# Optimization experiments

Measured on AMD Instinct MI355X. Metric: run time of the kernel, lower is better.

The kernel has to match this reference:

```python
import jax, jax.numpy as jnp
import numpy as np

N, E, D, B = 50000, 800000, 64, 64
NEXP, NC, EDIM, PDIM = 4, 10, 4, 100


def setup_inputs() -> dict:
    key = jax.random.key(0)
    ks = jax.random.split(key, 24)
    s = lambda f: 1.0 / np.sqrt(f)
    inp = {
        'x': jax.random.normal(ks[0], (N, D), jnp.float32),
        'edge_index': jax.random.randint(ks[1], (2, E), 0, N, jnp.int32),
        'edge_attr': jax.random.normal(ks[2], (E, EDIM), jnp.float32),
        'batch': jnp.sort(jax.random.randint(ks[3], (N,), 0, B, jnp.int32)),
        'ldxb_flag': jax.random.normal(ks[4], (B,), jnp.float32),
        # layer 1 params
        'w_edge1': jax.random.normal(ks[5], (D, EDIM)) * s(EDIM),
        'b_edge1': jnp.zeros((D,), jnp.float32),
        'w_ih1': jax.random.normal(ks[6], (3 * D, D)) * s(D),
        'w_hh1': jax.random.normal(ks[7], (3 * D, D)) * s(D),
        'b_ih1': jnp.zeros((3 * D,), jnp.float32),
        'b_hh1': jnp.zeros((3 * D,), jnp.float32),
        # layer 2 params
        'w_edge2': jax.random.normal(ks[8], (D, EDIM)) * s(EDIM),
        'b_edge2': jnp.zeros((D,), jnp.float32),
        'w_ih2': jax.random.normal(ks[9], (3 * D, D)) * s(D),
        'w_hh2': jax.random.normal(ks[10], (3 * D, D)) * s(D),
        'b_ih2': jnp.zeros((3 * D,), jnp.float32),
        'b_hh2': jnp.zeros((3 * D,), jnp.float32),
        # MoE
        'gate_w': jax.random.normal(ks[11], (NEXP, D)) * s(D),
        'gate_b': jnp.zeros((NEXP,), jnp.float32),
        'exp_w': jax.random.normal(ks[12], (NEXP, D, D)) * s(D),
        'exp_b': jnp.zeros((NEXP, D), jnp.float32),
        # heads
        'proj_w': jax.random.normal(ks[13], (PDIM, 1)),
        'proj_b': jnp.zeros((PDIM,), jnp.float32),
        'fc_w': jax.random.normal(ks[14], (NC, D + PDIM)) * s(D + PDIM),
        'fc_b': jnp.zeros((NC,), jnp.float32),
    }
    return inp


def _ggnn_layer(x, src, dst, eemb, w_ih, w_hh, b_ih, b_hh):
    # gather + scatter-add message passing (self-loops already in src/dst/eemb)
    msg = x[src] + eemb                       # [E+N, D]
    m = jnp.zeros_like(x).at[dst].add(msg)    # [N, D]
    # GRUCell(m, x): x is the hidden state
    gi = m @ w_ih.T + b_ih
    gh = x @ w_hh.T + b_hh
    i_r, i_z, i_n = jnp.split(gi, 3, axis=1)
    h_r, h_z, h_n = jnp.split(gh, 3, axis=1)
    r = jax.nn.sigmoid(i_r + h_r)
    z = jax.nn.sigmoid(i_z + h_z)
    n = jnp.tanh(i_n + r * h_n)
    return (1.0 - z) * n + z * x


def reference(x, edge_index, edge_attr, batch, ldxb_flag,
              w_edge1, b_edge1, w_ih1, w_hh1, b_ih1, b_hh1,
              w_edge2, b_edge2, w_ih2, w_hh2, b_ih2, b_hh2,
              gate_w, gate_b, exp_w, exp_b, proj_w, proj_b, fc_w, fc_b):
    n = x.shape[0]
    loop = jnp.arange(n, dtype=edge_index.dtype)
    src = jnp.concatenate([edge_index[0], loop])
    dst = jnp.concatenate([edge_index[1], loop])
    ea = jnp.concatenate([edge_attr, jnp.zeros((n, edge_attr.shape[1]), edge_attr.dtype)], axis=0)

    h = _ggnn_layer(x, src, dst, ea @ w_edge1.T + b_edge1, w_ih1, w_hh1, b_ih1, b_hh1)
    h = jax.nn.relu(h)
    h = _ggnn_layer(h, src, dst, ea @ w_edge2.T + b_edge2, w_ih2, w_hh2, b_ih2, b_hh2)
    h = jax.nn.relu(h)

    # soft MoE combine
    gw = jax.nn.softmax(h @ gate_w.T + gate_b, axis=1)            # [N, NEXP]
    eo = jax.nn.relu(jnp.einsum('nd,ehd->neh', h, exp_w) + exp_b)  # [N, NEXP, D]
    h = jnp.einsum('ne,neh->nh', gw, eo)                           # [N, D]

    # global mean pool per graph
    sums = jax.ops.segment_sum(h, batch, num_segments=B)
    cnts = jax.ops.segment_sum(jnp.ones((n,), h.dtype), batch, num_segments=B)
    graph_emb = sums / jnp.maximum(cnts, 1.0)[:, None]             # [B, D]

    flag = ldxb_flag[:, None] @ proj_w.T + proj_b                  # [B, 100]
    logits = jnp.concatenate([flag, graph_emb], axis=1) @ fc_w.T + fc_b
    return (graph_emb, graph_emb, logits)
```

## Files before the change

kernel.cpp:

```cpp
#include <hip/hip_runtime.h>
#include <stdint.h>


#define SUBCAP 8
#define OVF_MAX 32768
#define PS 16

typedef __bf16 bf16x8 __attribute__((ext_vector_type(8)));
typedef float floatx4 __attribute__((ext_vector_type(4)));
typedef unsigned short us8 __attribute__((ext_vector_type(8)));

__device__ __forceinline__ unsigned short f2bf(float f){
  union { float f; unsigned u; } c; c.f = f;
  unsigned r = c.u + 0x7FFFu + ((c.u >> 16) & 1u);
  return (unsigned short)(r >> 16);
}
__device__ __forceinline__ float bf2f(unsigned short u){
  union { unsigned u; float f; } c; c.u = ((unsigned)u) << 16; return c.f;
}
__device__ __forceinline__ float sigm(float x){ return 1.f/(1.f + __expf(-x)); }

__global__ void k_init(const float* __restrict__ x, unsigned short* __restrict__ x_bf,
                       const float* __restrict__ s0, const float* __restrict__ s1,
                       const float* __restrict__ s2, const float* __restrict__ s3,
                       const float* __restrict__ s4, const float* __restrict__ s5,
                       unsigned short* __restrict__ dst,
                       int* __restrict__ cur, int* __restrict__ ovfcnt,
                       int nTot, int N8){
  int i = blockIdx.x*blockDim.x + threadIdx.x;
  if (i < nTot) x_bf[i] = f2bf(x[i]);
  if (i < N8) cur[i] = 0;
  if (i == 0){ ovfcnt[0] = 0; }
  if (i >= 65792) return;
  const float* s; int off;
  if      (i < 12288){ s = s0; off = i; }
  else if (i < 24576){ s = s1; off = i - 12288; }
  else if (i < 36864){ s = s2; off = i - 24576; }
  else if (i < 49152){ s = s3; off = i - 36864; }
  else if (i < 49408){ s = s4; off = i - 49152; }
  else               { s = s5; off = i - 49408; }
  dst[i] = f2bf(s[off]);
}

__global__ void k_bucket(const int* __restrict__ ei, const float* __restrict__ ea,
                         int* __restrict__ cur, int4* __restrict__ bkt,
                         int* __restrict__ ovfcnt, int* __restrict__ ovf,
                         int E, int N){
  int base = (blockIdx.x*blockDim.x + threadIdx.x)*2;
  if (base >= E) return;
  int sub = blockIdx.x & 7;
  bool v1 = base + 1 < E;
  int2 ss = *(const int2*)(ei + base);
  int2 dd = *(const int2*)(ei + E + base);
  if (!v1){ dd.y = dd.x; ss.y = ss.x; }
  float4 a0 = *(const float4*)(ea + (size_t)base*4);
  float4 a1 = v1 ? *(const float4*)(ea + (size_t)(base+1)*4) : a0;
  size_t sb0 = (size_t)sub*N + dd.x;
  size_t sb1 = (size_t)sub*N + dd.y;
  int p0 = atomicAdd(&cur[sb0], 1);
  int p1 = v1 ? atomicAdd(&cur[sb1], 1) : SUBCAP;
  if (p0 < SUBCAP){
    int4 rec;
    rec.x = ss.x;
    rec.y = (int)((unsigned)f2bf(a0.x) | ((unsigned)f2bf(a0.y) << 16));
    rec.z = (int)((unsigned)f2bf(a0.z) | ((unsigned)f2bf(a0.w) << 16));
    rec.w = 0;
    bkt[sb0*SUBCAP + p0] = rec;
  } else {
    int o = atomicAdd(ovfcnt, 1);
    if (o < OVF_MAX) ovf[o] = base;
  }
  if (v1){
    if (p1 < SUBCAP){
      int4 rec;
      rec.x = ss.y;
      rec.y = (int)((unsigned)f2bf(a1.x) | ((unsigned)f2bf(a1.y) << 16));
      rec.z = (int)((unsigned)f2bf(a1.z) | ((unsigned)f2bf(a1.w) << 16));
      rec.w = 0;
      bkt[sb1*SUBCAP + p1] = rec;
    } else {
      int o = atomicAdd(ovfcnt, 1);
      if (o < OVF_MAX) ovf[o] = base + 1;
    }
  }
}

__global__ void __launch_bounds__(256) k_gather(
    const int* __restrict__ cur, const int4* __restrict__ bkt,
    const unsigned short* __restrict__ xbf,
    const float* __restrict__ w_edge, const float* __restrict__ b_edge,
    float* __restrict__ m, int N){
  int n = (int)(((long long)blockIdx.x*blockDim.x + threadIdx.x) >> 6);
  if (n >= N) return;
  int d = threadIdx.x & 63;
  int sub = d >> 3, k = d & 7;
  size_t sb = (size_t)sub*N + n;
  int myc = cur[sb];
  int contrib = (k == 0) ? myc : 0;
#pragma unroll
  for (int off = 1; off < 64; off <<= 1) contrib += __shfl_xor(contrib, off);
  int degAll = contrib;

  bool valid = k < min(myc, SUBCAP);
  int src = 0;
  float esx = 0.f, esy = 0.f, esz = 0.f, esw = 0.f;
  if (valid){
    int4 rec = bkt[sb*SUBCAP + k];
    src = rec.x;
    esx = bf2f((unsigned short)(rec.y      ));
    esy = bf2f((unsigned short)(rec.y >> 16));
    esz = bf2f((unsigned short)(rec.z      ));
    esw = bf2f((unsigned short)(rec.z >> 16));
  }

  float4 wv = *(const float4*)(w_edge + d*4);
  float acc = bf2f(xbf[(size_t)n*64 + d]) + (float)(degAll + 1) * b_edge[d];

  unsigned long long mm = __ballot(valid);
  while (mm){
    int l0 = (int)__builtin_ctzll(mm); mm &= mm - 1;
    int s0 = __shfl(src, l0);
    float a0 = bf2f(xbf[(size_t)s0*64 + d]);
    float a1 = 0.f, a2 = 0.f, a3 = 0.f;
    if (mm){
      int l1 = (int)__builtin_ctzll(mm); mm &= mm - 1;
      int s1 = __shfl(src, l1);
      a1 = bf2f(xbf[(size_t)s1*64 + d]);
      if (mm){
        int l2 = (int)__builtin_ctzll(mm); mm &= mm - 1;
        int s2 = __shfl(src, l2);
        a2 = bf2f(xbf[(size_t)s2*64 + d]);
        if (mm){
          int l3 = (int)__builtin_ctzll(mm); mm &= mm - 1;
          int s3 = __shfl(src, l3);
          a3 = bf2f(xbf[(size_t)s3*64 + d]);
        }
      }
    }
    acc += (a0 + a1) + (a2 + a3);
  }

#pragma unroll
  for (int off = 1; off < 64; off <<= 1){
    esx += __shfl_xor(esx, off);
    esy += __shfl_xor(esy, off);
    esz += __shfl_xor(esz, off);
    esw += __shfl_xor(esw, off);
  }
  acc += esx*wv.x + esy*wv.y + esz*wv.z + esw*wv.w;
  m[(size_t)n*64 + d] = acc;
}

__global__ void k_ovf(const int* __restrict__ ei, const float* __restrict__ ea,
                      const float* __restrict__ xin, const float* __restrict__ w_edge,
                      const int* __restrict__ ovf, const int* __restrict__ ovfcnt,
                      float* __restrict__ m, int E){
  int cnt = *ovfcnt; if (cnt > OVF_MAX) cnt = OVF_MAX;
  int nwaves = (gridDim.x * blockDim.x) >> 6;
  int wid = (int)((blockIdx.x*blockDim.x + threadIdx.x) >> 6);
  int d = threadIdx.x & 63;
  for (int k = wid; k < cnt; k += nwaves){
    int e = ovf[k];
    int s = ei[e], dst = ei[E + e];
    float4 v  = *(const float4*)(ea + (size_t)e*4);
    float4 wv = *(const float4*)(w_edge + d*4);
    float msg = xin[(size_t)s*64 + d] + v.x*wv.x + v.y*wv.y + v.z*wv.z + v.w*wv.w;
    atomicAdd(&m[(size_t)dst*64 + d], msg);
  }
}

__global__ void __launch_bounds__(256) k_gru(
    const float* __restrict__ m, const float* x,
    const unsigned short* __restrict__ xbf,
    const unsigned short* __restrict__ wih, const unsigned short* __restrict__ whh,
    const float* __restrict__ b_ih, const float* __restrict__ b_hh,
    float* out, unsigned short* out_bf, int tiles, int N){
  int wid = (int)(((long long)blockIdx.x*blockDim.x + threadIdx.x) >> 6);
  if (wid >= tiles) return;
  int lane = threadIdx.x & 63;
  int col = lane & 15, quad = lane >> 4;
  int na = wid*16 + col; if (na > N-1) na = N-1;

  bf16x8 am[2], ax[2];
#pragma unroll
  for (int ks = 0; ks < 2; ++ks){
    int kb = ks*32 + quad*8;
    const float4* mp = (const float4*)(m + (size_t)na*64 + kb);
    float4 lo = mp[0], hi = mp[1];
    us8 tm;
    tm[0]=f2bf(lo.x); tm[1]=f2bf(lo.y); tm[2]=f2bf(lo.z); tm[3]=f2bf(lo.w);
    tm[4]=f2bf(hi.x); tm[5]=f2bf(hi.y); tm[6]=f2bf(hi.z); tm[7]=f2bf(hi.w);
    am[ks] = __builtin_bit_cast(bf16x8, tm);
    ax[ks] = __builtin_bit_cast(bf16x8, *(const us8*)(xbf + (size_t)na*64 + kb));
  }

  floatx4 ai[12], ah[12];
#pragma unroll
  for (int nt = 0; nt < 12; ++nt){ ai[nt] = (floatx4)0.f; ah[nt] = (floatx4)0.f; }
#pragma unroll
  for (int nt = 0; nt < 12; ++nt){
    int r = nt*16 + col;
#pragma unroll
    for (int ks = 0; ks < 2; ++ks){
      int kb = ks*32 + quad*8;
      bf16x8 bi = __builtin_bit_cast(bf16x8, *(const us8*)(wih + (size_t)r*64 + kb));
      ai[nt] = __builtin_amdgcn_mfma_f32_16x16x32_bf16(am[ks], bi, ai[nt], 0,0,0);
      bf16x8 bh = __builtin_bit_cast(bf16x8, *(const us8*)(whh + (size_t)r*64 + kb));
      ah[nt] = __builtin_amdgcn_mfma_f32_16x16x32_bf16(ax[ks], bh, ah[nt], 0,0,0);
    }
  }

#pragma unroll
  for (int nt = 0; nt < 4; ++nt){
    int d = nt*16 + col;
    float bir = b_ih[d],      bhr = b_hh[d];
    float biz = b_ih[64+d],   bhz = b_hh[64+d];
    float bin = b_ih[128+d],  bhn = b_hh[128+d];
#pragma unroll
    for (int rg = 0; rg < 4; ++rg){
      int node = wid*16 + quad*4 + rg;
      if (node >= N) continue;
      float rr = sigm(ai[nt  ][rg] + bir + ah[nt  ][rg] + bhr);
      float zz = sigm(ai[nt+4][rg] + biz + ah[nt+4][rg] + bhz);
      float nn = tanhf(ai[nt+8][rg] + bin + rr*(ah[nt+8][rg] + bhn));
      float xv = x[(size_t)node*64 + d];
      float hv = fmaxf((1.f - zz)*nn + zz*xv, 0.f);
      out[(size_t)node*64 + d] = hv;
      out_bf[(size_t)node*64 + d] = f2bf(hv);
    }
  }
}

__global__ void __launch_bounds__(256) k_moe(
    const unsigned short* __restrict__ hbf,
    const unsigned short* __restrict__ gate_w, const float* __restrict__ gate_b,
    const unsigned short* __restrict__ exp_w,  const float* __restrict__ exp_b,
    float* __restrict__ v_out, int tiles, int N){
  __shared__ float gsm[4][16][4];
  int gwid = (int)(((long long)blockIdx.x*blockDim.x + threadIdx.x) >> 6);
  int w = threadIdx.x >> 6;
  int lane = threadIdx.x & 63;
  int col = lane & 15, quad = lane >> 4;
  bool active = gwid < tiles;

  floatx4 accg = (floatx4)0.f;
  floatx4 acce[4][4];
#pragma unroll
  for (int e=0;e<4;++e)
#pragma unroll
    for (int nt=0;nt<4;++nt) acce[e][nt] = (floatx4)0.f;

  if (active){
    int na = gwid*16 + col; if (na > N-1) na = N-1;
    bf16x8 a[2];
#pragma unroll
    for (int ks=0; ks<2; ++ks){
      int kb = ks*32 + quad*8;
      a[ks] = __builtin_bit_cast(bf16x8, *(const us8*)(hbf + (size_t)na*64 + kb));
      us8 braw = {0,0,0,0,0,0,0,0};
      if (col < 4) braw = *(const us8*)(gate_w + col*64 + kb);
      accg = __builtin_amdgcn_mfma_f32_16x16x32_bf16(a[ks], __builtin_bit_cast(bf16x8, braw), accg, 0,0,0);
    }
#pragma unroll
    for (int e=0;e<4;++e)
#pragma unroll
      for (int nt=0;nt<4;++nt)
#pragma unroll
        for (int ks=0;ks<2;++ks){
          int kb = ks*32 + quad*8;
          bf16x8 b = __builtin_bit_cast(bf16x8,
              *(const us8*)(exp_w + ((size_t)e*64 + nt*16 + col)*64 + kb));
          acce[e][nt] = __builtin_amdgcn_mfma_f32_16x16x32_bf16(a[ks], b, acce[e][nt], 0,0,0);
        }
    if (col < 4){
      float gb = gate_b[col];
#pragma unroll
      for (int rg=0;rg<4;++rg) gsm[w][quad*4+rg][col] = accg[rg] + gb;
    }
  }
  __syncthreads();
  if (!active) return;

#pragma unroll
  for (int rg=0; rg<4; ++rg){
    int nrow = quad*4 + rg;
    int node = gwid*16 + nrow;
    if (node >= N) continue;
    float g0=gsm[w][nrow][0], g1=gsm[w][nrow][1], g2=gsm[w][nrow][2], g3=gsm[w][nrow][3];
    float mx = fmaxf(fmaxf(g0,g1), fmaxf(g2,g3));
    float e0=__expf(g0-mx), e1=__expf(g1-mx), e2=__expf(g2-mx), e3=__expf(g3-mx);
    float inv = 1.f/(e0+e1+e2+e3);
    float w0=e0*inv, w1=e1*inv, w2=e2*inv, w3=e3*inv;
#pragma unroll
    for (int nt=0;nt<4;++nt){
      int o = nt*16 + col;
      float v = w0*fmaxf(acce[0][nt][rg] + exp_b[      o], 0.f)
              + w1*fmaxf(acce[1][nt][rg] + exp_b[ 64 + o], 0.f)
              + w2*fmaxf(acce[2][nt][rg] + exp_b[128 + o], 0.f)
              + w3*fmaxf(acce[3][nt][rg] + exp_b[192 + o], 0.f);
      v_out[(size_t)node*64 + o] = v;
    }
  }
}

__device__ __forceinline__ int lower_bound_i(const int* __restrict__ a, int n, int key){
  int lo = 0, hi = n;
  while (lo < hi){ int mid = (lo + hi) >> 1; if (a[mid] < key) lo = mid + 1; else hi = mid; }
  return lo;
}

__global__ void __launch_bounds__(256) k_pool(
    const float* __restrict__ v, const int* __restrict__ batch, int N,
    float* __restrict__ partial){
  __shared__ float red[4][64];
  int g = blockIdx.x / PS, s = blockIdx.x % PS;
  int t = threadIdx.x, d = t & 63, r = t >> 6;
  int start = lower_bound_i(batch, N, g);
  int end   = lower_bound_i(batch, N, g + 1);
  int len = end - start;
  int per = (len + PS - 1) / PS;
  int s0 = start + s*per;
  int s1 = s0 + per; if (s1 > end) s1 = end;
  float acc = 0.f;
  for (int i = s0 + r; i < s1; i += 4)
    acc += v[(size_t)i*64 + d];
  red[r][d] = acc;
  __syncthreads();
  if (r == 0)
    partial[(size_t)blockIdx.x*64 + d] = red[0][d] + red[1][d] + red[2][d] + red[3][d];
}

__global__ void __launch_bounds__(64) k_head(
    const float* __restrict__ partial, const int* __restrict__ batch, int N, int B,
    const float* __restrict__ ldxb,
    const float* __restrict__ proj_w, const float* __restrict__ proj_b,
    const float* __restrict__ fc_w, const float* __restrict__ fc_b,
    float* __restrict__ out){
  __shared__ float ges[64];
  int b = blockIdx.x, d = threadIdx.x;
  int start = lower_bound_i(batch, N, b);
  int end   = lower_bound_i(batch, N, b + 1);
  float sum = 0.f;
#pragma unroll
  for (int s = 0; s < PS; ++s)
    sum += partial[((size_t)b*PS + s)*64 + d];
  float ge = sum / fmaxf((float)(end - start), 1.f);
  ges[d] = ge;
  out[(size_t)b*64 + d]                = ge;
  out[(size_t)B*64 + (size_t)b*64 + d] = ge;
  __syncthreads();
  if (d < 10){
    float acc = fc_b[d];
    float fl = ldxb[b];
    const float* fr = fc_w + d*164;
    for (int p = 0; p < 100; ++p) acc += (fl*proj_w[p] + proj_b[p]) * fr[p];
    for (int dd = 0; dd < 64; ++dd) acc += ges[dd]*fr[100 + dd];
    out[(size_t)B*128 + (size_t)b*10 + d] = acc;
  }
}

extern "C" void kernel_launch(void* const* d_in, const int* in_sizes, int n_in,
                              void* d_out, int out_size, void* d_ws, size_t ws_size,
                              hipStream_t stream){
  const float* x      = (const float*)d_in[0];
  const int*   ei     = (const int*)d_in[1];
  const float* ea     = (const float*)d_in[2];
  const int*   batch  = (const int*)d_in[3];
  const float* ldxb   = (const float*)d_in[4];
  const float* w_edge1= (const float*)d_in[5];
  const float* b_edge1= (const float*)d_in[6];
  const float* w_ih1  = (const float*)d_in[7];
  const float* w_hh1  = (const float*)d_in[8];
  const float* b_ih1  = (const float*)d_in[9];
  const float* b_hh1  = (const float*)d_in[10];
  const float* w_edge2= (const float*)d_in[11];
  const float* b_edge2= (const float*)d_in[12];
  const float* w_ih2  = (const float*)d_in[13];
  const float* w_hh2  = (const float*)d_in[14];
  const float* b_ih2  = (const float*)d_in[15];
  const float* b_hh2  = (const float*)d_in[16];
  const float* gate_w = (const float*)d_in[17];
  const float* gate_b = (const float*)d_in[18];
  const float* exp_w  = (const float*)d_in[19];
  const float* exp_b  = (const float*)d_in[20];
  const float* proj_w = (const float*)d_in[21];
  const float* proj_b = (const float*)d_in[22];
  const float* fc_w   = (const float*)d_in[23];
  const float* fc_b   = (const float*)d_in[24];
  float* out = (float*)d_out;

  int N = in_sizes[0] / 64;
  int E = in_sizes[1] / 2;
  int B = in_sizes[4];
  int tiles = (N + 15) / 16;
  int nTot = N * 64;

  float*   m       = (float*)d_ws;
  float*   h       = m + (size_t)nTot;
  unsigned short* x_bf = (unsigned short*)(h + (size_t)nTot);
  unsigned short* h_bf = x_bf + (size_t)nTot;
  int4*    bkt     = (int4*)(h_bf + (size_t)nTot);
  int*     cur     = (int*)(bkt + (size_t)N*8*SUBCAP);
  int*     ovfcnt  = cur + (size_t)N*8;
  int*     ovf     = ovfcnt + 4;
  unsigned short* wbf = (unsigned short*)(ovf + OVF_MAX);
  float*   partial = (float*)(wbf + 65792);
  unsigned short* wih1bf = wbf;
  unsigned short* whh1bf = wbf + 12288;
  unsigned short* wih2bf = wbf + 24576;
  unsigned short* whh2bf = wbf + 36864;
  unsigned short* gatebf = wbf + 49152;
  unsigned short* expbf  = wbf + 49408;

  dim3 blk(256);
  int edgePairBlocks = (((E + 1)/2) + 255)/256;
  int nodeWaveBlocks = (N + 3)/4;
  int waveBlocks = (tiles + 3)/4;
  int N8 = N*8;
  int initMax = nTot > N8 ? nTot : N8; if (initMax < 65792) initMax = 65792;
  int initBlocks = (initMax + 255)/256;

  k_init<<<initBlocks, blk, 0, stream>>>(x, x_bf, w_ih1, w_hh1, w_ih2, w_hh2,
                                         gate_w, exp_w, wbf, cur, ovfcnt, nTot, N8);
  k_bucket<<<edgePairBlocks, blk, 0, stream>>>(ei, ea, cur, bkt, ovfcnt, ovf, E, N);
  k_gather<<<nodeWaveBlocks, blk, 0, stream>>>(cur, bkt, x_bf, w_edge1, b_edge1, m, N);
  k_ovf<<<64, blk, 0, stream>>>(ei, ea, x, w_edge1, ovf, ovfcnt, m, E);
  k_gru<<<waveBlocks, blk, 0, stream>>>(m, x, x_bf, wih1bf, whh1bf, b_ih1, b_hh1,
                                        h, h_bf, tiles, N);
  k_gather<<<nodeWaveBlocks, blk, 0, stream>>>(cur, bkt, h_bf, w_edge2, b_edge2, m, N);
  k_ovf<<<64, blk, 0, stream>>>(ei, ea, h, w_edge2, ovf, ovfcnt, m, E);
  k_gru<<<waveBlocks, blk, 0, stream>>>(m, h, h_bf, wih2bf, whh2bf, b_ih2, b_hh2,
                                        h, h_bf, tiles, N);
  k_moe<<<waveBlocks, blk, 0, stream>>>(h_bf, gatebf, gate_b, expbf, exp_b, m, tiles, N);
  k_pool<<<B*PS, blk, 0, stream>>>(m, batch, N, partial);
  k_head<<<B, 64, 0, stream>>>(partial, batch, N, B, ldxb, proj_w, proj_b, fc_w, fc_b, out);
}
```

Baseline: 369.2 us.

## Fold overflow edges into gather kernel and widen gather unroll to eight

The bucket kernel now writes self-contained overflow records (dst, src, packed bf16 edge attributes) instead of edge indices. Each gather wave scans the overflow list and adds any matching edges itself. This removes the separate atomic-based overflow kernel and its two launches. The gather loop also issues up to eight independent source-row loads per iteration instead of four, to expose more memory-level parallelism. In exchange, every node wave rereads the whole overflow list, and overflow messages now use bf16 features rather than fp32.

```diff
diff --git a/kernel.cpp b/kernel.cpp
--- a/kernel.cpp
+++ b/kernel.cpp
@@ -44,7 +44,7 @@
 
 __global__ void k_bucket(const int* __restrict__ ei, const float* __restrict__ ea,
                          int* __restrict__ cur, int4* __restrict__ bkt,
-                         int* __restrict__ ovfcnt, int* __restrict__ ovf,
+                         int* __restrict__ ovfcnt, int4* __restrict__ ovfrec,
                          int E, int N){
   int base = (blockIdx.x*blockDim.x + threadIdx.x)*2;
   if (base >= E) return;
@@ -59,28 +59,22 @@
   size_t sb1 = (size_t)sub*N + dd.y;
   int p0 = atomicAdd(&cur[sb0], 1);
   int p1 = v1 ? atomicAdd(&cur[sb1], 1) : SUBCAP;
+  int ea0_01 = (int)((unsigned)f2bf(a0.x) | ((unsigned)f2bf(a0.y) << 16));
+  int ea0_23 = (int)((unsigned)f2bf(a0.z) | ((unsigned)f2bf(a0.w) << 16));
   if (p0 < SUBCAP){
-    int4 rec;
-    rec.x = ss.x;
-    rec.y = (int)((unsigned)f2bf(a0.x) | ((unsigned)f2bf(a0.y) << 16));
-    rec.z = (int)((unsigned)f2bf(a0.z) | ((unsigned)f2bf(a0.w) << 16));
-    rec.w = 0;
-    bkt[sb0*SUBCAP + p0] = rec;
+    bkt[sb0*SUBCAP + p0] = make_int4(ss.x, ea0_01, ea0_23, 0);
   } else {
     int o = atomicAdd(ovfcnt, 1);
-    if (o < OVF_MAX) ovf[o] = base;
+    if (o < OVF_MAX) ovfrec[o] = make_int4(dd.x, ss.x, ea0_01, ea0_23);
   }
   if (v1){
+    int ea1_01 = (int)((unsigned)f2bf(a1.x) | ((unsigned)f2bf(a1.y) << 16));
+    int ea1_23 = (int)((unsigned)f2bf(a1.z) | ((unsigned)f2bf(a1.w) << 16));
     if (p1 < SUBCAP){
-      int4 rec;
-      rec.x = ss.y;
-      rec.y = (int)((unsigned)f2bf(a1.x) | ((unsigned)f2bf(a1.y) << 16));
-      rec.z = (int)((unsigned)f2bf(a1.z) | ((unsigned)f2bf(a1.w) << 16));
-      rec.w = 0;
-      bkt[sb1*SUBCAP + p1] = rec;
+      bkt[sb1*SUBCAP + p1] = make_int4(ss.y, ea1_01, ea1_23, 0);
     } else {
       int o = atomicAdd(ovfcnt, 1);
-      if (o < OVF_MAX) ovf[o] = base + 1;
+      if (o < OVF_MAX) ovfrec[o] = make_int4(dd.y, ss.y, ea1_01, ea1_23);
     }
   }
 }
@@ -89,6 +83,7 @@
     const int* __restrict__ cur, const int4* __restrict__ bkt,
     const unsigned short* __restrict__ xbf,
     const float* __restrict__ w_edge, const float* __restrict__ b_edge,
+    const int4* __restrict__ ovfrec, const int* __restrict__ ovfcnt,
     float* __restrict__ m, int N){
   int n = (int)(((long long)blockIdx.x*blockDim.x + threadIdx.x) >> 6);
   if (n >= N) return;
@@ -118,26 +113,24 @@
 
   unsigned long long mm = __ballot(valid);
   while (mm){
-    int l0 = (int)__builtin_ctzll(mm); mm &= mm - 1;
-    int s0 = __shfl(src, l0);
-    float a0 = bf2f(xbf[(size_t)s0*64 + d]);
-    float a1 = 0.f, a2 = 0.f, a3 = 0.f;
-    if (mm){
-      int l1 = (int)__builtin_ctzll(mm); mm &= mm - 1;
-      int s1 = __shfl(src, l1);
-      a1 = bf2f(xbf[(size_t)s1*64 + d]);
-      if (mm){
-        int l2 = (int)__builtin_ctzll(mm); mm &= mm - 1;
-        int s2 = __shfl(src, l2);
-        a2 = bf2f(xbf[(size_t)s2*64 + d]);
-        if (mm){
-          int l3 = (int)__builtin_ctzll(mm); mm &= mm - 1;
-          int s3 = __shfl(src, l3);
-          a3 = bf2f(xbf[(size_t)s3*64 + d]);
-        }
-      }
-    }
-    acc += (a0 + a1) + (a2 + a3);
+    int s0=-1,s1=-1,s2=-1,s3=-1,s4=-1,s5=-1,s6=-1,s7=-1;
+    { int l=(int)__builtin_ctzll(mm); mm&=mm-1; s0=__shfl(src,l); }
+    if (mm){ int l=(int)__builtin_ctzll(mm); mm&=mm-1; s1=__shfl(src,l); }
+    if (mm){ int l=(int)__builtin_ctzll(mm); mm&=mm-1; s2=__shfl(src,l); }
+    if (mm){ int l=(int)__builtin_ctzll(mm); mm&=mm-1; s3=__shfl(src,l); }
+    if (mm){ int l=(int)__builtin_ctzll(mm); mm&=mm-1; s4=__shfl(src,l); }
+    if (mm){ int l=(int)__builtin_ctzll(mm); mm&=mm-1; s5=__shfl(src,l); }
+    if (mm){ int l=(int)__builtin_ctzll(mm); mm&=mm-1; s6=__shfl(src,l); }
+    if (mm){ int l=(int)__builtin_ctzll(mm); mm&=mm-1; s7=__shfl(src,l); }
+    float a0 = (s0>=0) ? bf2f(xbf[(size_t)s0*64 + d]) : 0.f;
+    float a1 = (s1>=0) ? bf2f(xbf[(size_t)s1*64 + d]) : 0.f;
+    float a2 = (s2>=0) ? bf2f(xbf[(size_t)s2*64 + d]) : 0.f;
+    float a3 = (s3>=0) ? bf2f(xbf[(size_t)s3*64 + d]) : 0.f;
+    float a4 = (s4>=0) ? bf2f(xbf[(size_t)s4*64 + d]) : 0.f;
+    float a5 = (s5>=0) ? bf2f(xbf[(size_t)s5*64 + d]) : 0.f;
+    float a6 = (s6>=0) ? bf2f(xbf[(size_t)s6*64 + d]) : 0.f;
+    float a7 = (s7>=0) ? bf2f(xbf[(size_t)s7*64 + d]) : 0.f;
+    acc += ((a0 + a1) + (a2 + a3)) + ((a4 + a5) + (a6 + a7));
   }
 
 #pragma unroll
@@ -148,25 +141,25 @@
     esw += __shfl_xor(esw, off);
   }
   acc += esx*wv.x + esy*wv.y + esz*wv.z + esw*wv.w;
+
+  int oc = *ovfcnt; if (oc > OVF_MAX) oc = OVF_MAX;
+  for (int base = 0; base < oc; base += 64){
+    int4 r = make_int4(-1, 0, 0, 0);
+    if (base + d < oc) r = ovfrec[base + d];
+    unsigned long long match = __ballot(r.x == n);
+    while (match){
+      int l = (int)__builtin_ctzll(match); match &= match - 1;
+      int osrc = __shfl(r.y, l);
+      int oe01 = __shfl(r.z, l);
+      int oe23 = __shfl(r.w, l);
+      acc += bf2f(xbf[(size_t)osrc*64 + d])
+           + bf2f((unsigned short)(oe01      ))*wv.x
+           + bf2f((unsigned short)(oe01 >> 16))*wv.y
+           + bf2f((unsigned short)(oe23      ))*wv.z
+           + bf2f((unsigned short)(oe23 >> 16))*wv.w;
+    }
+  }
   m[(size_t)n*64 + d] = acc;
-}
-
-__global__ void k_ovf(const int* __restrict__ ei, const float* __restrict__ ea,
-                      const float* __restrict__ xin, const float* __restrict__ w_edge,
-                      const int* __restrict__ ovf, const int* __restrict__ ovfcnt,
-                      float* __restrict__ m, int E){
-  int cnt = *ovfcnt; if (cnt > OVF_MAX) cnt = OVF_MAX;
-  int nwaves = (gridDim.x * blockDim.x) >> 6;
-  int wid = (int)((blockIdx.x*blockDim.x + threadIdx.x) >> 6);
-  int d = threadIdx.x & 63;
-  for (int k = wid; k < cnt; k += nwaves){
-    int e = ovf[k];
-    int s = ei[e], dst = ei[E + e];
-    float4 v  = *(const float4*)(ea + (size_t)e*4);
-    float4 wv = *(const float4*)(w_edge + d*4);
-    float msg = xin[(size_t)s*64 + d] + v.x*wv.x + v.y*wv.y + v.z*wv.z + v.w*wv.w;
-    atomicAdd(&m[(size_t)dst*64 + d], msg);
-  }
 }
 
 __global__ void __launch_bounds__(256) k_gru(
@@ -402,8 +395,8 @@
   int4*    bkt     = (int4*)(h_bf + (size_t)nTot);
   int*     cur     = (int*)(bkt + (size_t)N*8*SUBCAP);
   int*     ovfcnt  = cur + (size_t)N*8;
-  int*     ovf     = ovfcnt + 4;
-  unsigned short* wbf = (unsigned short*)(ovf + OVF_MAX);
+  int4*    ovfrec  = (int4*)(ovfcnt + 4);
+  unsigned short* wbf = (unsigned short*)(ovfrec + OVF_MAX);
   float*   partial = (float*)(wbf + 65792);
   unsigned short* wih1bf = wbf;
   unsigned short* whh1bf = wbf + 12288;
@@ -422,13 +415,13 @@
 
   k_init<<<initBlocks, blk, 0, stream>>>(x, x_bf, w_ih1, w_hh1, w_ih2, w_hh2,
                                          gate_w, exp_w, wbf, cur, ovfcnt, nTot, N8);
-  k_bucket<<<edgePairBlocks, blk, 0, stream>>>(ei, ea, cur, bkt, ovfcnt, ovf, E, N);
-  k_gather<<<nodeWaveBlocks, blk, 0, stream>>>(cur, bkt, x_bf, w_edge1, b_edge1, m, N);
-  k_ovf<<<64, blk, 0, stream>>>(ei, ea, x, w_edge1, ovf, ovfcnt, m, E);
+  k_bucket<<<edgePairBlocks, blk, 0, stream>>>(ei, ea, cur, bkt, ovfcnt, ovfrec, E, N);
+  k_gather<<<nodeWaveBlocks, blk, 0, stream>>>(cur, bkt, x_bf, w_edge1, b_edge1,
+                                               ovfrec, ovfcnt, m, N);
   k_gru<<<waveBlocks, blk, 0, stream>>>(m, x, x_bf, wih1bf, whh1bf, b_ih1, b_hh1,
                                         h, h_bf, tiles, N);
-  k_gather<<<nodeWaveBlocks, blk, 0, stream>>>(cur, bkt, h_bf, w_edge2, b_edge2, m, N);
-  k_ovf<<<64, blk, 0, stream>>>(ei, ea, h, w_edge2, ovf, ovfcnt, m, E);
+  k_gather<<<nodeWaveBlocks, blk, 0, stream>>>(cur, bkt, h_bf, w_edge2, b_edge2,
+                                               ovfrec, ovfcnt, m, N);
   k_gru<<<waveBlocks, blk, 0, stream>>>(m, h, h_bf, wih2bf, whh2bf, b_ih2, b_hh2,
                                         h, h_bf, tiles, N);
   k_moe<<<waveBlocks, blk, 0, stream>>>(h_bf, gatebf, gate_b, expbf, exp_b, m, tiles, N);
```

New measurement: 414.7 us. 1.12x slower.
